# Kernel tuning notes

Measured on AMD Instinct MI355X. Metric: run time of the kernel, lower is better.

## Reference

```python
import jax, jax.numpy as jnp
import numpy as np

T, B, D, H, NQ = 512, 128, 512, 64, 64  # seq_len, batch, input_dim, hidden_dim == n_qubits
EPS = 1e-5

def setup_inputs() -> dict:
    key = jax.random.key(0)
    ks = jax.random.split(key, 11)
    s = 0.05
    return {
        "inputs": jax.random.normal(ks[0], (T, B, D), jnp.float32),
        "W0": jax.random.normal(ks[1], (4, NQ, D + H), jnp.float32) * s,
        "b0": jax.random.normal(ks[2], (4, NQ), jnp.float32) * s,
        "th0": jax.random.normal(ks[3], (4, NQ), jnp.float32) * s,
        "g0": jnp.ones((H,), jnp.float32),
        "be0": jnp.zeros((H,), jnp.float32),
        "W1": jax.random.normal(ks[4], (4, NQ, H + H), jnp.float32) * s,
        "b1": jax.random.normal(ks[5], (4, NQ), jnp.float32) * s,
        "th1": jax.random.normal(ks[6], (4, NQ), jnp.float32) * s,
        "g1": jnp.ones((H,), jnp.float32),
        "be1": jnp.zeros((H,), jnp.float32),
    }

def _qlstm_layer(x, W, b, th, gamma, beta):
    # x: [T, B, Din]. Faithful to source: h_prev = c_prev = 0 at EVERY timestep
    # (the torch code never writes back `states` inside the time loop), so all
    # timesteps are independent and fully vectorized.
    zeros_h = jnp.zeros(x.shape[:-1] + (H,), x.dtype)
    combined = jnp.concatenate([x, zeros_h], axis=-1)           # [T,B,Din+H]
    # 4 gate linears stacked on leading axis g: forget, input, update, output
    z = jnp.einsum('tbk,gnk->gtbn', combined, W) + b[:, None, None, :]
    # quantum circuit closed form: RX(z_i+th_i) per qubit + CNOT ladder + <Z_k>
    #   => cumprod_{i<=k} cos(z_i + th_i)
    q = jnp.cumprod(jnp.cos(z + th[:, None, None, :]), axis=-1)  # [4,T,B,NQ]
    sg = jax.nn.sigmoid(q)
    i_g = sg[1]
    g_g = jnp.tanh(sg[2])
    o_g = sg[3]
    # c = f * c_prev + i * g, with c_prev == 0  (f gate has no effect)
    c = i_g * g_g                                                # [T,B,H]
    h = o_g * jnp.tanh(c)
    mu = jnp.mean(h, axis=-1, keepdims=True)
    var = jnp.mean((h - mu) ** 2, axis=-1, keepdims=True)
    h_ln = (h - mu) * jax.lax.rsqrt(var + EPS) * gamma + beta
    return h_ln, c

def reference(inputs, W0, b0, th0, g0, be0, W1, b1, th1, g1, be1):
    h0, c0 = _qlstm_layer(inputs, W0, b0, th0, g0, be0)  # layer 0 (no dropout: p=0)
    h1, c1 = _qlstm_layer(h0, W1, b1, th1, g1, be1)      # layer 1
    outputs = h1                                          # [T,B,H]
    # new_states = states at the last timestep: [(h_ln, c)] per layer
    return (outputs, h0[-1], c0[-1], h1[-1], c1[-1])
```

## Files before the change

kernel.cpp:

```cpp
#include <hip/hip_runtime.h>
#include <hip/hip_bf16.h>

typedef __attribute__((ext_vector_type(8))) short bf16x8;
typedef __attribute__((ext_vector_type(4))) float f32x4;

#define T_SEQ   512
#define B_BATCH 128
#define H_DIM   64
#define MB      64
#define AS_STRIDE 136
#define ZS_STRIDE 193
#define HS_STRIDE 68
#define LASTROW ((T_SEQ - 1) * B_BATCH)

#define W0H 0
#define W0M 98304
#define W0L 196608
#define W1H 294912
#define W1M 307200
#define W1L 319488

__device__ __forceinline__ void tsplit(float f, unsigned& h, unsigned& m, unsigned& l) {
    unsigned uf = __builtin_bit_cast(unsigned, f);
    h = uf >> 16;
    float hf = __builtin_bit_cast(float, uf & 0xFFFF0000u);
    float r1 = f - hf;
    unsigned u1 = __builtin_bit_cast(unsigned, r1);
    m = u1 >> 16;
    float mf = __builtin_bit_cast(float, u1 & 0xFFFF0000u);
    float r2 = r1 - mf;
    l = __builtin_bit_cast(unsigned, r2) >> 16;
}

__device__ __forceinline__ void tsplit2(float a, float b,
                                        unsigned& ph, unsigned& pm, unsigned& pl) {
    unsigned ha, ma, la, hb, mb, lb;
    tsplit(a, ha, ma, la);
    tsplit(b, hb, mb, lb);
    ph = ha | (hb << 16);
    pm = ma | (mb << 16);
    pl = la | (lb << 16);
}

__device__ __forceinline__ f32x4 mfma6(bf16x8 ah, bf16x8 am, bf16x8 al,
                                       bf16x8 bh, bf16x8 bm, bf16x8 bl, f32x4 c) {
    c = __builtin_amdgcn_mfma_f32_16x16x32_bf16(ah, bh, c, 0, 0, 0);
    c = __builtin_amdgcn_mfma_f32_16x16x32_bf16(ah, bm, c, 0, 0, 0);
    c = __builtin_amdgcn_mfma_f32_16x16x32_bf16(am, bh, c, 0, 0, 0);
    c = __builtin_amdgcn_mfma_f32_16x16x32_bf16(ah, bl, c, 0, 0, 0);
    c = __builtin_amdgcn_mfma_f32_16x16x32_bf16(al, bh, c, 0, 0, 0);
    c = __builtin_amdgcn_mfma_f32_16x16x32_bf16(am, bm, c, 0, 0, 0);
    return c;
}

__device__ __forceinline__ float acc_sigmoid(float x) {
    float e = expf(-x);
    float d = 1.0f + e;
    float r = __builtin_amdgcn_rcpf(d);
    r = r * (2.0f - d * r);
    return r;
}

__global__ __launch_bounds__(256) void presplit_w(const float* __restrict__ W0,
                                                  const float* __restrict__ W1,
                                                  short* __restrict__ ws) {
    int i = blockIdx.x * 256 + threadIdx.x;
    if (i < 98304) {
        int r = i >> 9, k = i & 511;
        unsigned h, m, l;
        tsplit(W0[(r + 64) * 576 + k], h, m, l);
        ws[W0H + i] = (short)h;
        ws[W0M + i] = (short)m;
        ws[W0L + i] = (short)l;
    } else if (i < 110592) {
        int j = i - 98304;
        int r = j >> 6, k = j & 63;
        unsigned h, m, l;
        tsplit(W1[(r + 64) * 128 + k], h, m, l);
        ws[W1H + j] = (short)h;
        ws[W1M + j] = (short)m;
        ws[W1L + j] = (short)l;
    }
}

__global__ __launch_bounds__(256) void qlstm_fused(
    const float* __restrict__ x,
    const float* __restrict__ b0,
    const float* __restrict__ th0,
    const float* __restrict__ g0,
    const float* __restrict__ be0,
    const float* __restrict__ b1,
    const float* __restrict__ th1,
    const float* __restrict__ g1,
    const float* __restrict__ be1,
    const short* __restrict__ wsp,
    float* __restrict__ out)
{
    __shared__ __align__(16) char lds[71168];
    short* ah = (short*)lds;
    short* am = ah + 64 * AS_STRIDE;
    short* al = am + 64 * AS_STRIDE;
    float* zs  = (float*)lds;
    float* hs  = (float*)(lds + 52224);
    float* bt0 = (float*)(lds + 69632);
    float* bt1 = bt0 + 192;

    const int tid = threadIdx.x;
    const long rowbase = (long)blockIdx.x * MB;

    float* out0 = out;
    float* out1 = out + (long)T_SEQ * B_BATCH * H_DIM;
    float* out2 = out1 + B_BATCH * H_DIM;
    float* out3 = out2 + B_BATCH * H_DIM;
    float* out4 = out3 + B_BATCH * H_DIM;

    if (tid < 192) {
        bt0[tid] = b0[64 + tid] + th0[64 + tid];
        bt1[tid] = b1[64 + tid] + th1[64 + tid];
    }

    const int lane = tid & 63;
    const int wave = tid >> 6;
    const int ln   = lane & 15;
    const int quad = lane >> 4;
    const int cw   = wave * 48;

    int brow0[3], brow1[3];
    for (int nt = 0; nt < 3; ++nt) {
        int gc = cw + nt * 16 + ln;
        brow0[nt] = gc * 512;
        brow1[nt] = gc * 64;
    }

    f32x4 acc[4][3];
    for (int mt = 0; mt < 4; ++mt)
        for (int nt = 0; nt < 3; ++nt)
            acc[mt][nt] = (f32x4){0.f, 0.f, 0.f, 0.f};

    for (int kc = 0; kc < 512; kc += 128) {
        for (int pass = 0; pass < 4; ++pass) {
            int e  = pass * 256 + tid;
            int r  = e >> 4;
            int k8 = (e & 15) << 3;
            const float* xp = x + (rowbase + r) * 512 + kc + k8;
            float4 f0 = *(const float4*)xp;
            float4 f1 = *(const float4*)(xp + 4);
            uint4 Ph, Pm, Pl;
            tsplit2(f0.x, f0.y, Ph.x, Pm.x, Pl.x);
            tsplit2(f0.z, f0.w, Ph.y, Pm.y, Pl.y);
            tsplit2(f1.x, f1.y, Ph.z, Pm.z, Pl.z);
            tsplit2(f1.z, f1.w, Ph.w, Pm.w, Pl.w);
            int ao = r * AS_STRIDE + k8;
            *(uint4*)(ah + ao) = Ph;
            *(uint4*)(am + ao) = Pm;
            *(uint4*)(al + ao) = Pl;
        }
        __syncthreads();
        for (int k0 = 0; k0 < 128; k0 += 32) {
            int ka = k0 + quad * 8;
            bf16x8 Ah[4], Am[4], Al[4];
            for (int mt = 0; mt < 4; ++mt) {
                int ao = (mt * 16 + ln) * AS_STRIDE + ka;
                Ah[mt] = *(const bf16x8*)(ah + ao);
                Am[mt] = *(const bf16x8*)(am + ao);
                Al[mt] = *(const bf16x8*)(al + ao);
            }
            for (int nt = 0; nt < 3; ++nt) {
                int bo = brow0[nt] + kc + ka;
                bf16x8 Bh = *(const bf16x8*)(wsp + W0H + bo);
                bf16x8 Bm = *(const bf16x8*)(wsp + W0M + bo);
                bf16x8 Bl = *(const bf16x8*)(wsp + W0L + bo);
                for (int mt = 0; mt < 4; ++mt)
                    acc[mt][nt] = mfma6(Ah[mt], Am[mt], Al[mt], Bh, Bm, Bl, acc[mt][nt]);
            }
        }
        __syncthreads();
    }

    for (int mt = 0; mt < 4; ++mt)
        for (int nt = 0; nt < 3; ++nt)
            for (int i = 0; i < 4; ++i) {
                int row = mt * 16 + quad * 4 + i;
                int col = cw + nt * 16 + ln;
                zs[row * ZS_STRIDE + col] = acc[mt][nt][i];
            }
    __syncthreads();

    if (tid < 192) {
        int gi = tid >> 6;
        int r  = tid & 63;
        float* zrow = zs + r * ZS_STRIDE + gi * 64;
        const float* btg = bt0 + gi * 64;
        float p = 1.0f;
        for (int n = 0; n < 64; ++n) {
            p *= cosf(zrow[n] + btg[n]);
            zrow[n] = p;
        }
    }
    __syncthreads();

    {
        int r = tid >> 2;
        int j = tid & 3;
        long tbrow = rowbase + r;
        bool lastt = (tbrow >= LASTROW);
        int bidx = (int)(tbrow - LASTROW);
        const float* zr = zs + r * ZS_STRIDE;
        float h[16];
        float s = 0.f;
        for (int i = 0; i < 16; ++i) {
            int n = j * 16 + i;
            float q1 = zr[n];
            float q2 = zr[64 + n];
            float q3 = zr[128 + n];
            float ig = acc_sigmoid(q1);
            float gg = tanhf(acc_sigmoid(q2));
            float og = acc_sigmoid(q3);
            float c  = ig * gg;
            float hv = og * tanhf(c);
            h[i] = hv;
            s += hv;
            if (lastt) out2[bidx * 64 + n] = c;
        }
        s += __shfl_xor(s, 1);  s += __shfl_xor(s, 2);
        float mu = s * (1.0f / 64.0f);
        float s2 = 0.f;
        for (int i = 0; i < 16; ++i) {
            float d = h[i] - mu;
            s2 += d * d;
        }
        s2 += __shfl_xor(s2, 1); s2 += __shfl_xor(s2, 2);
        float var = s2 * (1.0f / 64.0f);
        float rs  = rsqrtf(var + 1e-5f);
        for (int i = 0; i < 16; ++i) {
            int n = j * 16 + i;
            float hl = (h[i] - mu) * rs * g0[n] + be0[n];
            hs[r * HS_STRIDE + n] = hl;
            if (lastt) out1[bidx * 64 + n] = hl;
        }
    }
    __syncthreads();

    f32x4 acc2[4][3];
    for (int mt = 0; mt < 4; ++mt)
        for (int nt = 0; nt < 3; ++nt)
            acc2[mt][nt] = (f32x4){0.f, 0.f, 0.f, 0.f};
    for (int k0 = 0; k0 < 64; k0 += 32) {
        int ka = k0 + quad * 8;
        bf16x8 Ah[4], Am[4], Al[4];
        for (int mt = 0; mt < 4; ++mt) {
            const float* p = hs + (mt * 16 + ln) * HS_STRIDE + ka;
            float4 f0 = *(const float4*)p;
            float4 f1 = *(const float4*)(p + 4);
            uint4 Ph, Pm, Pl;
            tsplit2(f0.x, f0.y, Ph.x, Pm.x, Pl.x);
            tsplit2(f0.z, f0.w, Ph.y, Pm.y, Pl.y);
            tsplit2(f1.x, f1.y, Ph.z, Pm.z, Pl.z);
            tsplit2(f1.z, f1.w, Ph.w, Pm.w, Pl.w);
            Ah[mt] = __builtin_bit_cast(bf16x8, Ph);
            Am[mt] = __builtin_bit_cast(bf16x8, Pm);
            Al[mt] = __builtin_bit_cast(bf16x8, Pl);
        }
        for (int nt = 0; nt < 3; ++nt) {
            int bo = brow1[nt] + ka;
            bf16x8 Bh = *(const bf16x8*)(wsp + W1H + bo);
            bf16x8 Bm = *(const bf16x8*)(wsp + W1M + bo);
            bf16x8 Bl = *(const bf16x8*)(wsp + W1L + bo);
            for (int mt = 0; mt < 4; ++mt)
                acc2[mt][nt] = mfma6(Ah[mt], Am[mt], Al[mt], Bh, Bm, Bl, acc2[mt][nt]);
        }
    }
    for (int mt = 0; mt < 4; ++mt)
        for (int nt = 0; nt < 3; ++nt)
            for (int i = 0; i < 4; ++i) {
                int row = mt * 16 + quad * 4 + i;
                int col = cw + nt * 16 + ln;
                zs[row * ZS_STRIDE + col] = acc2[mt][nt][i];
            }
    __syncthreads();

    if (tid < 192) {
        int gi = tid >> 6;
        int r  = tid & 63;
        float* zrow = zs + r * ZS_STRIDE + gi * 64;
        const float* btg = bt1 + gi * 64;
        float p = 1.0f;
        for (int n = 0; n < 64; ++n) {
            p *= cosf(zrow[n] + btg[n]);
            zrow[n] = p;
        }
    }
    __syncthreads();

    {
        int r = tid >> 2;
        int j = tid & 3;
        long tbrow = rowbase + r;
        bool lastt = (tbrow >= LASTROW);
        int bidx = (int)(tbrow - LASTROW);
        const float* zr = zs + r * ZS_STRIDE;
        float h[16];
        float s = 0.f;
        for (int i = 0; i < 16; ++i) {
            int n = j * 16 + i;
            float q1 = zr[n];
            float q2 = zr[64 + n];
            float q3 = zr[128 + n];
            float ig = acc_sigmoid(q1);
            float gg = tanhf(acc_sigmoid(q2));
            float og = acc_sigmoid(q3);
            float c  = ig * gg;
            float hv = og * tanhf(c);
            h[i] = hv;
            s += hv;
            if (lastt) out4[bidx * 64 + n] = c;
        }
        s += __shfl_xor(s, 1);  s += __shfl_xor(s, 2);
        float mu = s * (1.0f / 64.0f);
        float s2 = 0.f;
        for (int i = 0; i < 16; ++i) {
            float d = h[i] - mu;
            s2 += d * d;
        }
        s2 += __shfl_xor(s2, 1); s2 += __shfl_xor(s2, 2);
        float var = s2 * (1.0f / 64.0f);
        float rs  = rsqrtf(var + 1e-5f);
        float o4[16];
        for (int i = 0; i < 16; ++i)
            o4[i] = (h[i] - mu) * rs * g1[j * 16 + i] + be1[j * 16 + i];
        float* dst = out0 + tbrow * 64 + j * 16;
        for (int i4 = 0; i4 < 4; ++i4)
            *(float4*)(dst + i4 * 4) = *(float4*)(o4 + i4 * 4);
        if (lastt) {
            float* dst3 = out3 + (long)bidx * 64 + j * 16;
            for (int i4 = 0; i4 < 4; ++i4)
                *(float4*)(dst3 + i4 * 4) = *(float4*)(o4 + i4 * 4);
        }
    }
}

extern "C" void kernel_launch(void* const* d_in, const int* in_sizes, int n_in,
                              void* d_out, int out_size, void* d_ws, size_t ws_size,
                              hipStream_t stream) {
    const float* x   = (const float*)d_in[0];
    const float* W0  = (const float*)d_in[1];
    const float* b0  = (const float*)d_in[2];
    const float* th0 = (const float*)d_in[3];
    const float* g0  = (const float*)d_in[4];
    const float* be0 = (const float*)d_in[5];
    const float* W1  = (const float*)d_in[6];
    const float* b1  = (const float*)d_in[7];
    const float* th1 = (const float*)d_in[8];
    const float* g1  = (const float*)d_in[9];
    const float* be1 = (const float*)d_in[10];
    short* wsp = (short*)d_ws;

    presplit_w<<<dim3(432), dim3(256), 0, stream>>>(W0, W1, wsp);
    qlstm_fused<<<dim3(1024), dim3(256), 0, stream>>>(
        x, b0, th0, g0, be0, b1, th1, g1, be1, wsp, (float*)d_out);
}
```

Baseline: 328.7 us.

## Halve row tile and parallelize cumprod with wave-level shuffle scans

After: 408.7 us. +24.3%, slower.

```diff
diff --git a/kernel.cpp b/kernel.cpp
--- a/kernel.cpp
+++ b/kernel.cpp
@@ -7,7 +7,7 @@
 #define T_SEQ   512
 #define B_BATCH 128
 #define H_DIM   64
-#define MB      64
+#define MB      32
 #define AS_STRIDE 136
 #define ZS_STRIDE 193
 #define HS_STRIDE 68
@@ -59,6 +59,19 @@
     float r = __builtin_amdgcn_rcpf(d);
     r = r * (2.0f - d * r);
     return r;
+}
+
+__device__ __forceinline__ float scan_prod(float v, int lane) {
+    for (int d = 1; d < 64; d <<= 1) {
+        float t = __shfl_up(v, d);
+        v *= (lane >= d) ? t : 1.0f;
+    }
+    return v;
+}
+
+__device__ __forceinline__ float wave_sum(float v) {
+    for (int d = 1; d < 64; d <<= 1) v += __shfl_xor(v, d);
+    return v;
 }
 
 __global__ __launch_bounds__(256) void presplit_w(const float* __restrict__ W0,
@@ -96,14 +109,12 @@
     const short* __restrict__ wsp,
     float* __restrict__ out)
 {
-    __shared__ __align__(16) char lds[71168];
+    __shared__ __align__(16) char lds[34816];
     short* ah = (short*)lds;
-    short* am = ah + 64 * AS_STRIDE;
-    short* al = am + 64 * AS_STRIDE;
-    float* zs  = (float*)lds;
-    float* hs  = (float*)(lds + 52224);
-    float* bt0 = (float*)(lds + 69632);
-    float* bt1 = bt0 + 192;
+    short* am = ah + MB * AS_STRIDE;
+    short* al = am + MB * AS_STRIDE;
+    float* zs = (float*)lds;
+    float* hs = (float*)(lds + 26112);
 
     const int tid = threadIdx.x;
     const long rowbase = (long)blockIdx.x * MB;
@@ -114,17 +125,21 @@
     float* out3 = out2 + B_BATCH * H_DIM;
     float* out4 = out3 + B_BATCH * H_DIM;
 
-    if (tid < 192) {
-        bt0[tid] = b0[64 + tid] + th0[64 + tid];
-        bt1[tid] = b1[64 + tid] + th1[64 + tid];
-    }
-
     const int lane = tid & 63;
     const int wave = tid >> 6;
     const int ln   = lane & 15;
     const int quad = lane >> 4;
     const int cw   = wave * 48;
 
+    const float bt0a = b0[64  + lane] + th0[64  + lane];
+    const float bt0b = b0[128 + lane] + th0[128 + lane];
+    const float bt0c = b0[192 + lane] + th0[192 + lane];
+    const float bt1a = b1[64  + lane] + th1[64  + lane];
+    const float bt1b = b1[128 + lane] + th1[128 + lane];
+    const float bt1c = b1[192 + lane] + th1[192 + lane];
+    const float g0v = g0[lane], be0v = be0[lane];
+    const float g1v = g1[lane], be1v = be1[lane];
+
     int brow0[3], brow1[3];
     for (int nt = 0; nt < 3; ++nt) {
         int gc = cw + nt * 16 + ln;
@@ -132,13 +147,13 @@
         brow1[nt] = gc * 64;
     }
 
-    f32x4 acc[4][3];
-    for (int mt = 0; mt < 4; ++mt)
+    f32x4 acc[2][3];
+    for (int mt = 0; mt < 2; ++mt)
         for (int nt = 0; nt < 3; ++nt)
             acc[mt][nt] = (f32x4){0.f, 0.f, 0.f, 0.f};
 
     for (int kc = 0; kc < 512; kc += 128) {
-        for (int pass = 0; pass < 4; ++pass) {
+        for (int pass = 0; pass < 2; ++pass) {
             int e  = pass * 256 + tid;
             int r  = e >> 4;
             int k8 = (e & 15) << 3;
@@ -158,8 +173,8 @@
         __syncthreads();
         for (int k0 = 0; k0 < 128; k0 += 32) {
             int ka = k0 + quad * 8;
-            bf16x8 Ah[4], Am[4], Al[4];
-            for (int mt = 0; mt < 4; ++mt) {
+            bf16x8 Ah[2], Am[2], Al[2];
+            for (int mt = 0; mt < 2; ++mt) {
                 int ao = (mt * 16 + ln) * AS_STRIDE + ka;
                 Ah[mt] = *(const bf16x8*)(ah + ao);
                 Am[mt] = *(const bf16x8*)(am + ao);
@@ -170,14 +185,14 @@
                 bf16x8 Bh = *(const bf16x8*)(wsp + W0H + bo);
                 bf16x8 Bm = *(const bf16x8*)(wsp + W0M + bo);
                 bf16x8 Bl = *(const bf16x8*)(wsp + W0L + bo);
-                for (int mt = 0; mt < 4; ++mt)
+                for (int mt = 0; mt < 2; ++mt)
                     acc[mt][nt] = mfma6(Ah[mt], Am[mt], Al[mt], Bh, Bm, Bl, acc[mt][nt]);
             }
         }
         __syncthreads();
     }
 
-    for (int mt = 0; mt < 4; ++mt)
+    for (int mt = 0; mt < 2; ++mt)
         for (int nt = 0; nt < 3; ++nt)
             for (int i = 0; i < 4; ++i) {
                 int row = mt * 16 + quad * 4 + i;
@@ -186,72 +201,46 @@
             }
     __syncthreads();
 
-    if (tid < 192) {
-        int gi = tid >> 6;
-        int r  = tid & 63;
-        float* zrow = zs + r * ZS_STRIDE + gi * 64;
-        const float* btg = bt0 + gi * 64;
-        float p = 1.0f;
-        for (int n = 0; n < 64; ++n) {
-            p *= cosf(zrow[n] + btg[n]);
-            zrow[n] = p;
+    for (int p = 0; p < 8; ++p) {
+        int row = wave * 8 + p;
+        const float* zr = zs + row * ZS_STRIDE;
+        float c1 = cosf(zr[lane]        + bt0a);
+        float c2 = cosf(zr[64  + lane]  + bt0b);
+        float c3 = cosf(zr[128 + lane]  + bt0c);
+        float q1 = scan_prod(c1, lane);
+        float q2 = scan_prod(c2, lane);
+        float q3 = scan_prod(c3, lane);
+        float ig = acc_sigmoid(q1);
+        float gg = tanhf(acc_sigmoid(q2));
+        float og = acc_sigmoid(q3);
+        float c  = ig * gg;
+        float hv = og * tanhf(c);
+        float mu = wave_sum(hv) * (1.0f / 64.0f);
+        float d  = hv - mu;
+        float var = wave_sum(d * d) * (1.0f / 64.0f);
+        float rs  = rsqrtf(var + 1e-5f);
+        float hl  = d * rs * g0v + be0v;
+        hs[row * HS_STRIDE + lane] = hl;
+        long tbrow = rowbase + row;
+        if (tbrow >= LASTROW) {
+            int bidx = (int)(tbrow - LASTROW);
+            out1[bidx * 64 + lane] = hl;
+            out2[bidx * 64 + lane] = c;
         }
     }
     __syncthreads();
 
-    {
-        int r = tid >> 2;
-        int j = tid & 3;
-        long tbrow = rowbase + r;
-        bool lastt = (tbrow >= LASTROW);
-        int bidx = (int)(tbrow - LASTROW);
-        const float* zr = zs + r * ZS_STRIDE;
-        float h[16];
-        float s = 0.f;
-        for (int i = 0; i < 16; ++i) {
-            int n = j * 16 + i;
-            float q1 = zr[n];
-            float q2 = zr[64 + n];
-            float q3 = zr[128 + n];
-            float ig = acc_sigmoid(q1);
-            float gg = tanhf(acc_sigmoid(q2));
-            float og = acc_sigmoid(q3);
-            float c  = ig * gg;
-            float hv = og * tanhf(c);
-            h[i] = hv;
-            s += hv;
-            if (lastt) out2[bidx * 64 + n] = c;
-        }
-        s += __shfl_xor(s, 1);  s += __shfl_xor(s, 2);
-        float mu = s * (1.0f / 64.0f);
-        float s2 = 0.f;
-        for (int i = 0; i < 16; ++i) {
-            float d = h[i] - mu;
-            s2 += d * d;
-        }
-        s2 += __shfl_xor(s2, 1); s2 += __shfl_xor(s2, 2);
-        float var = s2 * (1.0f / 64.0f);
-        float rs  = rsqrtf(var + 1e-5f);
-        for (int i = 0; i < 16; ++i) {
-            int n = j * 16 + i;
-            float hl = (h[i] - mu) * rs * g0[n] + be0[n];
-            hs[r * HS_STRIDE + n] = hl;
-            if (lastt) out1[bidx * 64 + n] = hl;
-        }
-    }
-    __syncthreads();
-
-    f32x4 acc2[4][3];
-    for (int mt = 0; mt < 4; ++mt)
+    f32x4 acc2[2][3];
+    for (int mt = 0; mt < 2; ++mt)
         for (int nt = 0; nt < 3; ++nt)
             acc2[mt][nt] = (f32x4){0.f, 0.f, 0.f, 0.f};
     for (int k0 = 0; k0 < 64; k0 += 32) {
         int ka = k0 + quad * 8;
-        bf16x8 Ah[4], Am[4], Al[4];
-        for (int mt = 0; mt < 4; ++mt) {
-            const float* p = hs + (mt * 16 + ln) * HS_STRIDE + ka;
-            float4 f0 = *(const float4*)p;
-            float4 f1 = *(const float4*)(p + 4);
+        bf16x8 Ah[2], Am[2], Al[2];
+        for (int mt = 0; mt < 2; ++mt) {
+            const float* ptr = hs + (mt * 16 + ln) * HS_STRIDE + ka;
+            float4 f0 = *(const float4*)ptr;
+            float4 f1 = *(const float4*)(ptr + 4);
             uint4 Ph, Pm, Pl;
             tsplit2(f0.x, f0.y, Ph.x, Pm.x, Pl.x);
             tsplit2(f0.z, f0.w, Ph.y, Pm.y, Pl.y);
@@ -266,11 +255,11 @@
             bf16x8 Bh = *(const bf16x8*)(wsp + W1H + bo);
             bf16x8 Bm = *(const bf16x8*)(wsp + W1M + bo);
             bf16x8 Bl = *(const bf16x8*)(wsp + W1L + bo);
-            for (int mt = 0; mt < 4; ++mt)
+            for (int mt = 0; mt < 2; ++mt)
                 acc2[mt][nt] = mfma6(Ah[mt], Am[mt], Al[mt], Bh, Bm, Bl, acc2[mt][nt]);
         }
     }
-    for (int mt = 0; mt < 4; ++mt)
+    for (int mt = 0; mt < 2; ++mt)
         for (int nt = 0; nt < 3; ++nt)
             for (int i = 0; i < 4; ++i) {
                 int row = mt * 16 + quad * 4 + i;
@@ -279,62 +268,31 @@
             }
     __syncthreads();
 
-    if (tid < 192) {
-        int gi = tid >> 6;
-        int r  = tid & 63;
-        float* zrow = zs + r * ZS_STRIDE + gi * 64;
-        const float* btg = bt1 + gi * 64;
-        float p = 1.0f;
-        for (int n = 0; n < 64; ++n) {
-            p *= cosf(zrow[n] + btg[n]);
-            zrow[n] = p;
-        }
-    }
-    __syncthreads();
-
-    {
-        int r = tid >> 2;
-        int j = tid & 3;
-        long tbrow = rowbase + r;
-        bool lastt = (tbrow >= LASTROW);
-        int bidx = (int)(tbrow - LASTROW);
-        const float* zr = zs + r * ZS_STRIDE;
-        float h[16];
-        float s = 0.f;
-        for (int i = 0; i < 16; ++i) {
-            int n = j * 16 + i;
-            float q1 = zr[n];
-            float q2 = zr[64 + n];
-            float q3 = zr[128 + n];
-            float ig = acc_sigmoid(q1);
-            float gg = tanhf(acc_sigmoid(q2));
-            float og = acc_sigmoid(q3);
-            float c  = ig * gg;
-            float hv = og * tanhf(c);
-            h[i] = hv;
-            s += hv;
-            if (lastt) out4[bidx * 64 + n] = c;
-        }
-        s += __shfl_xor(s, 1);  s += __shfl_xor(s, 2);
-        float mu = s * (1.0f / 64.0f);
-        float s2 = 0.f;
-        for (int i = 0; i < 16; ++i) {
-            float d = h[i] - mu;
-            s2 += d * d;
-        }
-        s2 += __shfl_xor(s2, 1); s2 += __shfl_xor(s2, 2);
-        float var = s2 * (1.0f / 64.0f);
+    for (int p = 0; p < 8; ++p) {
+        int row = wave * 8 + p;
+        const float* zr = zs + row * ZS_STRIDE;
+        float c1 = cosf(zr[lane]        + bt1a);
+        float c2 = cosf(zr[64  + lane]  + bt1b);
+        float c3 = cosf(zr[128 + lane]  + bt1c);
+        float q1 = scan_prod(c1, lane);
+        float q2 = scan_prod(c2, lane);
+        float q3 = scan_prod(c3, lane);
+        float ig = acc_sigmoid(q1);
+        float gg = tanhf(acc_sigmoid(q2));
+        float og = acc_sigmoid(q3);
+        float c  = ig * gg;
+        float hv = og * tanhf(c);
+        float mu = wave_sum(hv) * (1.0f / 64.0f);
+        float d  = hv - mu;
+        float var = wave_sum(d * d) * (1.0f / 64.0f);
         float rs  = rsqrtf(var + 1e-5f);
-        float o4[16];
-        for (int i = 0; i < 16; ++i)
-            o4[i] = (h[i] - mu) * rs * g1[j * 16 + i] + be1[j * 16 + i];
-        float* dst = out0 + tbrow * 64 + j * 16;
-        for (int i4 = 0; i4 < 4; ++i4)
-            *(float4*)(dst + i4 * 4) = *(float4*)(o4 + i4 * 4);
-        if (lastt) {
-            float* dst3 = out3 + (long)bidx * 64 + j * 16;
-            for (int i4 = 0; i4 < 4; ++i4)
-                *(float4*)(dst3 + i4 * 4) = *(float4*)(o4 + i4 * 4);
+        float hl  = d * rs * g1v + be1v;
+        long tbrow = rowbase + row;
+        out0[tbrow * 64 + lane] = hl;
+        if (tbrow >= LASTROW) {
+            int bidx = (int)(tbrow - LASTROW);
+            out3[bidx * 64 + lane] = hl;
+            out4[bidx * 64 + lane] = c;
         }
     }
 }
@@ -356,6 +314,6 @@
     short* wsp = (short*)d_ws;
 
     presplit_w<<<dim3(432), dim3(256), 0, stream>>>(W0, W1, wsp);
-    qlstm_fused<<<dim3(1024), dim3(256), 0, stream>>>(
+    qlstm_fused<<<dim3(2048), dim3(256), 0, stream>>>(
         x, b0, th0, g0, be0, b1, th1, g1, be1, wsp, (float*)d_out);
 }
```
